# Kernel optimization log

Measured on AMD Instinct MI355X. Metric: run time of the kernel, lower is better.

The kernel has to match this reference:

```python
import jax, jax.numpy as jnp
import numpy as np

N_HEADS = 8
KEY_DIM = 64
MEM_DIM = 64
HEAD_DIM = 64
IN_DIM = 256
OUT_DIM = 256


def setup_inputs() -> dict:
    key = jax.random.key(0)
    ks = jax.random.split(key, 7)
    x = jax.random.normal(ks[0], (8, IN_DIM, 64, 64), dtype=jnp.float32)
    # learned params
    key_p = jax.random.uniform(ks[1], (N_HEADS, KEY_DIM, MEM_DIM), dtype=jnp.float32)
    memory = jax.random.uniform(ks[2], (N_HEADS, MEM_DIM, HEAD_DIM), dtype=jnp.float32) * 0.5 - 0.25
    w_in = jax.random.normal(ks[3], (N_HEADS * KEY_DIM, IN_DIM), dtype=jnp.float32) * (1.0 / np.sqrt(IN_DIM))
    b_in = jax.random.normal(ks[4], (N_HEADS * KEY_DIM,), dtype=jnp.float32) * 0.01
    w_out = jax.random.normal(ks[5], (OUT_DIM, N_HEADS * HEAD_DIM), dtype=jnp.float32) * (1.0 / np.sqrt(N_HEADS * HEAD_DIM))
    b_out = jax.random.normal(ks[6], (OUT_DIM,), dtype=jnp.float32) * 0.01
    return {"x": x, "key_p": key_p, "memory": memory, "w_in": w_in, "b_in": b_in, "w_out": w_out, "b_out": b_out}


def reference(x, key_p, memory, w_in, b_in, w_out, b_out):
    B, _, H, W = x.shape
    # 1x1 conv projection: [B, n_heads*key_dim, H, W]
    out = jnp.einsum('oc,bchw->bohw', w_in, x) + b_in[None, :, None, None]
    # split heads: b (k n) h w -> b n k h w  (einops '(c m)' with m=n_heads => c is outer)
    out = out.reshape(B, KEY_DIM, N_HEADS, H, W).transpose(0, 2, 1, 3, 4)
    # per-head key matmul over key_dim -> memory_dim
    out = jnp.einsum('nkm,bnkhw->bnmhw', key_p, out)
    out = jax.nn.softmax(out, axis=2)
    # per-head memory matmul over memory_dim -> head_dim
    out = jnp.einsum('nmd,bnmhw->bndhw', memory, out)
    # merge heads: b n d h w -> b (d n) h w  (einops 'b m c h w -> b (m c) h w' with m=heads... wait)
    # einops 'b m c h w -> b (m c) h w': m (heads) is outer -> transpose then reshape
    out = out.reshape(B, N_HEADS * HEAD_DIM, H, W)
    # final 1x1 conv
    out = jnp.einsum('oc,bchw->bohw', w_out, out) + b_out[None, :, None, None]
    return out
```

## Files before the change

kernel.cpp:

```cpp
#include <hip/hip_runtime.h>


typedef _Float16 half8 __attribute__((ext_vector_type(8)));
typedef _Float16 half4 __attribute__((ext_vector_type(4)));
typedef _Float16 half2v __attribute__((ext_vector_type(2)));
typedef float float4v __attribute__((ext_vector_type(4)));

__global__ __launch_bounds__(256) void fold_all(
    const float* __restrict__ key_p, const float* __restrict__ w_in,
    const float* __restrict__ b_in, const float* __restrict__ w_out,
    const float* __restrict__ memory,
    _Float16* __restrict__ Aswz, _Float16* __restrict__ Mswz, float* __restrict__ bb)
{
    __shared__ float sv[512];
    __shared__ float red[64];
    const int blk = blockIdx.x;
    const int t = threadIdx.x;

    if (blk < 512) {
        const int row = blk, n = row >> 6, m = row & 63;
        if (t < 64) sv[t] = key_p[n * 4096 + t * 64 + m];
        __syncthreads();
        const int c = t;
        float v = 0.f;
        #pragma unroll 8
        for (int k = 0; k < 64; ++k)
            v = fmaf(sv[k], w_in[(k * 8 + n) * 256 + c], v);
        int R = row >> 4, s = c >> 5, i = c & 7;
        int l = (row & 15) + 16 * ((c >> 3) & 3);
        Aswz[(((R * 8 + s) * 64 + l) << 3) + i] = (_Float16)v;
        if (t < 64) red[t] = sv[t] * b_in[t * 8 + n];
        __syncthreads();
        if (t == 0) {
            float s2 = 0.f;
            for (int k = 0; k < 64; ++k) s2 += red[k];
            bb[row] = s2;
        }
    } else {
        const int o = blk - 512;
        sv[t]       = w_out[o * 512 + t];
        sv[256 + t] = w_out[o * 512 + 256 + t];
        __syncthreads();
        #pragma unroll
        for (int hh = 0; hh < 2; ++hh) {
            int col = t + hh * 256, n = col >> 6, m = col & 63;
            const float4* mrow = (const float4*)(memory + n * 4096 + m * 64);
            const float4* wrow = (const float4*)(sv + n * 64);
            float v = 0.f;
            #pragma unroll
            for (int qd = 0; qd < 16; ++qd) {
                float4 a = mrow[qd], w = wrow[qd];
                v += a.x * w.x + a.y * w.y + a.z * w.z + a.w * w.w;
            }
            int R2 = o >> 4, s = col >> 5, i = col & 7;
            int l = (o & 15) + 16 * ((col >> 3) & 3);
            Mswz[(((R2 * 16 + s) * 64 + l) << 3) + i] = (_Float16)v;
        }
    }
}

#define XS_STRIDE 264

__global__ __launch_bounds__(256, 2) void fused_main(
    const float* __restrict__ x, const _Float16* __restrict__ Aswz,
    const float* __restrict__ bb, const _Float16* __restrict__ Mswz,
    const float* __restrict__ b_out, float* __restrict__ out)
{
    __shared__ _Float16 S[32768];

    const int t  = threadIdx.x;
    const int w  = t >> 6;
    const int l  = t & 63;
    const int q  = l >> 4;
    const int lp = l & 15;
    const int wg  = blockIdx.x;
    const int b   = wg >> 6;
    const int hw0 = (wg & 63) * 64;
    const float* xb = x + (size_t)b * 256 * 4096 + hw0;

    #pragma unroll
    for (int i = 0; i < 8; ++i) {
        int u  = i * 256 + t;
        int cp = u & 127;
        int qq = u >> 7;
        int c0 = cp * 2, p4 = qq * 4;
        const float* px = xb + (size_t)c0 * 4096 + p4;
        float4 v0 = *(const float4*)(px);
        float4 v1 = *(const float4*)(px + 4096);
        *(half2v*)(&S[(p4 + 0) * XS_STRIDE + c0]) = half2v{(_Float16)v0.x, (_Float16)v1.x};
        *(half2v*)(&S[(p4 + 1) * XS_STRIDE + c0]) = half2v{(_Float16)v0.y, (_Float16)v1.y};
        *(half2v*)(&S[(p4 + 2) * XS_STRIDE + c0]) = half2v{(_Float16)v0.z, (_Float16)v1.z};
        *(half2v*)(&S[(p4 + 3) * XS_STRIDE + c0]) = half2v{(_Float16)v0.w, (_Float16)v1.w};
    }
    __syncthreads();

    float4v acc[8][4];
    #pragma unroll
    for (int r = 0; r < 8; ++r)
        #pragma unroll
        for (int c = 0; c < 4; ++c) acc[r][c] = float4v{0.f, 0.f, 0.f, 0.f};

    const half8* Ag = (const half8*)Aswz;
    for (int s = 0; s < 8; ++s) {
        half8 bf[4];
        #pragma unroll
        for (int c = 0; c < 4; ++c)
            bf[c] = *(const half8*)(&S[(c * 16 + lp) * XS_STRIDE + s * 32 + q * 8]);
        half8 af[8];
        #pragma unroll
        for (int r = 0; r < 8; ++r)
            af[r] = Ag[((w * 8 + r) * 8 + s) * 64 + l];
        #pragma unroll
        for (int r = 0; r < 8; ++r)
            #pragma unroll
            for (int c = 0; c < 4; ++c)
                acc[r][c] = __builtin_amdgcn_mfma_f32_16x16x32_f16(af[r], bf[c], acc[r][c], 0, 0, 0);
    }

    #pragma unroll
    for (int r = 0; r < 8; ++r) {
        float4v bbv = *(const float4v*)(bb + w * 128 + r * 16 + q * 4);
        #pragma unroll
        for (int c = 0; c < 4; ++c)
            #pragma unroll
            for (int j = 0; j < 4; ++j) acc[r][c][j] += bbv[j];
    }

    __syncthreads();

    #pragma unroll
    for (int h = 0; h < 2; ++h) {
        #pragma unroll
        for (int c = 0; c < 4; ++c) {
            float mx = -1e30f;
            #pragma unroll
            for (int rr = 0; rr < 4; ++rr) {
                int r = h * 4 + rr;
                #pragma unroll
                for (int j = 0; j < 4; ++j) mx = fmaxf(mx, acc[r][c][j]);
            }
            mx = fmaxf(mx, __shfl_xor(mx, 16, 64));
            mx = fmaxf(mx, __shfl_xor(mx, 32, 64));
            float sum = 0.f;
            #pragma unroll
            for (int rr = 0; rr < 4; ++rr) {
                int r = h * 4 + rr;
                #pragma unroll
                for (int j = 0; j < 4; ++j) {
                    float e = __expf(acc[r][c][j] - mx);
                    acc[r][c][j] = e;
                    sum += e;
                }
            }
            sum += __shfl_xor(sum, 16, 64);
            sum += __shfl_xor(sum, 32, 64);
            float inv = 1.f / sum;
            #pragma unroll
            for (int rr = 0; rr < 4; ++rr) {
                int r = h * 4 + rr;
                int s2 = w * 4 + (r >> 1);
                int lq = ((r & 1) * 2 + (q >> 1)) * 16 + lp;
                int i0 = (q & 1) * 4;
                half4 pv = {(_Float16)(acc[r][c][0] * inv), (_Float16)(acc[r][c][1] * inv),
                            (_Float16)(acc[r][c][2] * inv), (_Float16)(acc[r][c][3] * inv)};
                *(half4*)(&S[(((s2 * 4 + c) * 64) + lq) * 8 + i0]) = pv;
            }
        }
    }
    __syncthreads();

    float4v acc2[4][4];
    #pragma unroll
    for (int r = 0; r < 4; ++r)
        #pragma unroll
        for (int c = 0; c < 4; ++c) acc2[r][c] = float4v{0.f, 0.f, 0.f, 0.f};

    const half8* Mg = (const half8*)Mswz;
    for (int s2 = 0; s2 < 16; ++s2) {
        half8 bf2[4];
        #pragma unroll
        for (int c = 0; c < 4; ++c)
            bf2[c] = *(const half8*)(&S[(((s2 * 4 + c) * 64) + l) * 8]);
        half8 af2[4];
        #pragma unroll
        for (int r = 0; r < 4; ++r)
            af2[r] = Mg[((w * 4 + r) * 16 + s2) * 64 + l];
        #pragma unroll
        for (int r = 0; r < 4; ++r)
            #pragma unroll
            for (int c = 0; c < 4; ++c)
                acc2[r][c] = __builtin_amdgcn_mfma_f32_16x16x32_f16(af2[r], bf2[c], acc2[r][c], 0, 0, 0);
    }

    #pragma unroll
    for (int r = 0; r < 4; ++r) {
        int ob = w * 64 + r * 16 + q * 4;
        float4v bo = *(const float4v*)(b_out + ob);
        #pragma unroll
        for (int j = 0; j < 4; ++j) {
            float* orow = out + ((size_t)b * 256 + ob + j) * 4096 + hw0;
            #pragma unroll
            for (int c = 0; c < 4; ++c)
                orow[c * 16 + lp] = acc2[r][c][j] + bo[j];
        }
    }
}

extern "C" void kernel_launch(void* const* d_in, const int* in_sizes, int n_in,
                              void* d_out, int out_size, void* d_ws, size_t ws_size,
                              hipStream_t stream) {
    (void)in_sizes; (void)n_in; (void)ws_size; (void)out_size;
    const float* x      = (const float*)d_in[0];
    const float* key_p  = (const float*)d_in[1];
    const float* memory = (const float*)d_in[2];
    const float* w_in   = (const float*)d_in[3];
    const float* b_in   = (const float*)d_in[4];
    const float* w_out  = (const float*)d_in[5];
    const float* b_out  = (const float*)d_in[6];
    float* out = (float*)d_out;

    _Float16* Aswz = (_Float16*)d_ws;
    _Float16* Mswz = Aswz + 512 * 256;
    float*    bb   = (float*)(Mswz + 256 * 512);

    fold_all<<<768, 256, 0, stream>>>(key_p, w_in, b_in, w_out, memory, Aswz, Mswz, bb);
    fused_main<<<512, 256, 0, stream>>>(x, Aswz, bb, Mswz, b_out, out);
}
```

Before: 120.2 us.

## Prefetch MFMA weight fragments one step ahead and remap x-tile load indexing

The weight fragments for both MFMA loops are now loaded one k-step ahead through register double-buffering, with the first fragment issued before the barrier, so global load latency can overlap the MFMAs and the shared-memory staging. The x staging loop's thread-to-element mapping is swapped so neighbouring threads read consecutive pixels within a channel row, which gives more coalesced global reads at the cost of different LDS write bank patterns. The fold kernel's inner loop unroll goes from 8 to 16. Fully unrolling the loops and holding double fragments raises register pressure under launch_bounds(256,2), which could cause spills.

```diff
diff --git a/kernel.cpp b/kernel.cpp
--- a/kernel.cpp
+++ b/kernel.cpp
@@ -23,7 +23,7 @@
         __syncthreads();
         const int c = t;
         float v = 0.f;
-        #pragma unroll 8
+        #pragma unroll 16
         for (int k = 0; k < 64; ++k)
             v = fmaf(sv[k], w_in[(k * 8 + n) * 256 + c], v);
         int R = row >> 4, s = c >> 5, i = c & 7;
@@ -81,8 +81,8 @@
     #pragma unroll
     for (int i = 0; i < 8; ++i) {
         int u  = i * 256 + t;
-        int cp = u & 127;
-        int qq = u >> 7;
+        int qq = u & 15;
+        int cp = u >> 4;
         int c0 = cp * 2, p4 = qq * 4;
         const float* px = xb + (size_t)c0 * 4096 + p4;
         float4 v0 = *(const float4*)(px);
@@ -92,6 +92,13 @@
         *(half2v*)(&S[(p4 + 2) * XS_STRIDE + c0]) = half2v{(_Float16)v0.z, (_Float16)v1.z};
         *(half2v*)(&S[(p4 + 3) * XS_STRIDE + c0]) = half2v{(_Float16)v0.w, (_Float16)v1.w};
     }
+
+    const half8* Ag = (const half8*)Aswz;
+    half8 af[8];
+    #pragma unroll
+    for (int r = 0; r < 8; ++r)
+        af[r] = Ag[((w * 8 + r) * 8 + 0) * 64 + l];
+
     __syncthreads();
 
     float4v acc[8][4];
@@ -100,21 +107,27 @@
         #pragma unroll
         for (int c = 0; c < 4; ++c) acc[r][c] = float4v{0.f, 0.f, 0.f, 0.f};
 
-    const half8* Ag = (const half8*)Aswz;
+    #pragma unroll
     for (int s = 0; s < 8; ++s) {
+        half8 afn[8];
+        if (s < 7) {
+            #pragma unroll
+            for (int r = 0; r < 8; ++r)
+                afn[r] = Ag[((w * 8 + r) * 8 + s + 1) * 64 + l];
+        }
         half8 bf[4];
         #pragma unroll
         for (int c = 0; c < 4; ++c)
             bf[c] = *(const half8*)(&S[(c * 16 + lp) * XS_STRIDE + s * 32 + q * 8]);
-        half8 af[8];
-        #pragma unroll
-        for (int r = 0; r < 8; ++r)
-            af[r] = Ag[((w * 8 + r) * 8 + s) * 64 + l];
         #pragma unroll
         for (int r = 0; r < 8; ++r)
             #pragma unroll
             for (int c = 0; c < 4; ++c)
                 acc[r][c] = __builtin_amdgcn_mfma_f32_16x16x32_f16(af[r], bf[c], acc[r][c], 0, 0, 0);
+        if (s < 7) {
+            #pragma unroll
+            for (int r = 0; r < 8; ++r) af[r] = afn[r];
+        }
     }
 
     #pragma unroll
@@ -167,6 +180,13 @@
             }
         }
     }
+
+    const half8* Mg = (const half8*)Mswz;
+    half8 af2[4];
+    #pragma unroll
+    for (int r = 0; r < 4; ++r)
+        af2[r] = Mg[((w * 4 + r) * 16 + 0) * 64 + l];
+
     __syncthreads();
 
     float4v acc2[4][4];
@@ -175,21 +195,27 @@
         #pragma unroll
         for (int c = 0; c < 4; ++c) acc2[r][c] = float4v{0.f, 0.f, 0.f, 0.f};
 
-    const half8* Mg = (const half8*)Mswz;
+    #pragma unroll
     for (int s2 = 0; s2 < 16; ++s2) {
+        half8 af2n[4];
+        if (s2 < 15) {
+            #pragma unroll
+            for (int r = 0; r < 4; ++r)
+                af2n[r] = Mg[((w * 4 + r) * 16 + s2 + 1) * 64 + l];
+        }
         half8 bf2[4];
         #pragma unroll
         for (int c = 0; c < 4; ++c)
             bf2[c] = *(const half8*)(&S[(((s2 * 4 + c) * 64) + l) * 8]);
-        half8 af2[4];
-        #pragma unroll
-        for (int r = 0; r < 4; ++r)
-            af2[r] = Mg[((w * 4 + r) * 16 + s2) * 64 + l];
         #pragma unroll
         for (int r = 0; r < 4; ++r)
             #pragma unroll
             for (int c = 0; c < 4; ++c)
                 acc2[r][c] = __builtin_amdgcn_mfma_f32_16x16x32_f16(af2[r], bf2[c], acc2[r][c], 0, 0, 0);
+        if (s2 < 15) {
+            #pragma unroll
+            for (int r = 0; r < 4; ++r) af2[r] = af2n[r];
+        }
     }
 
     #pragma unroll
```

New measurement: 129.6 us. 7.8% more time.
